# Kernel optimization log

Measured on AMD Instinct MI355X. Metric: run time of the kernel, lower is better.

## Reference

```python
import jax, jax.numpy as jnp
import numpy as np

NUM_HEADS = 4
NUM_GROUPS = 32
EPS = 1e-5


def group_norm(x, gamma, beta):
    B, C, H, W = x.shape
    g = x.reshape(B, NUM_GROUPS, C // NUM_GROUPS, H, W)
    mean = g.mean(axis=(2, 3, 4), keepdims=True)
    var = g.var(axis=(2, 3, 4), keepdims=True)
    g = (g - mean) * jax.lax.rsqrt(var + EPS)
    x = g.reshape(B, C, H, W)
    return x * gamma[None, :, None, None] + beta[None, :, None, None]


def setup_inputs() -> dict:
    key = jax.random.key(0)
    ks = jax.random.split(key, 7)
    B, C, H, W = 16, 256, 32, 32
    x = jax.random.normal(ks[0], (B, C, H, W), dtype=jnp.float32)
    gn_gamma = jnp.ones((C,), dtype=jnp.float32)
    gn_beta = jnp.zeros((C,), dtype=jnp.float32)
    s = 1.0 / np.sqrt(C)
    qkv_w = jax.random.normal(ks[1], (3 * C, C), dtype=jnp.float32) * s
    qkv_b = jnp.zeros((3 * C,), dtype=jnp.float32)
    proj_w = jax.random.normal(ks[2], (C, C), dtype=jnp.float32) * s
    proj_b = jnp.zeros((C,), dtype=jnp.float32)
    return {"x": x, "gn_gamma": gn_gamma, "gn_beta": gn_beta,
            "qkv_w": qkv_w, "qkv_b": qkv_b, "proj_w": proj_w, "proj_b": proj_b}


def reference(x, gn_gamma, gn_beta, qkv_w, qkv_b, proj_w, proj_b):
    B, C, H, W = x.shape
    nh = NUM_HEADS
    d = C // nh
    N = H * W

    h = group_norm(x, gn_gamma, gn_beta)
    # 1x1 conv == channel matmul
    qkv = jnp.einsum('bchw,oc->bohw', h, qkv_w) + qkv_b[None, :, None, None]
    qkv = qkv.reshape(B, 3, nh, d, N)
    q, k, v = qkv[:, 0], qkv[:, 1], qkv[:, 2]  # each [B, nh, d, N]

    scale = 1.0 / jnp.sqrt(jnp.asarray(d, dtype=x.dtype))
    attn = jnp.einsum('bhdn,bhdm->bhnm', q, k) * scale  # [B, nh, N, N]
    attn = jax.nn.softmax(attn, axis=-1)
    out = jnp.einsum('bhnm,bhdm->bhdn', attn, v)  # [B, nh, d, N]
    out = out.reshape(B, C, H, W)

    out = jnp.einsum('bchw,oc->bohw', out, proj_w) + proj_b[None, :, None, None]
    return x + out
```

## Files before the change

### kernel.cpp

```cpp
#include <hip/hip_runtime.h>
#include <math.h>

typedef unsigned short u16;
typedef unsigned int u32;
typedef __attribute__((ext_vector_type(8))) short s16x8;
typedef __attribute__((ext_vector_type(4))) float f32x4;

#define NB 16
#define NN 1024
#define GN_EPS 1e-5f

static __device__ __forceinline__ u16 f2bf(float f) {
    union { float f; u32 u; } v; v.f = f;
    return (u16)((v.u + 0x8000u) >> 16);
}
static __device__ __forceinline__ u32 pk2(float a, float b) {
    union { float f; u32 u; } A, B; A.f = a; B.f = b;
    return __builtin_amdgcn_perm(A.u + 0x8000u, B.u + 0x8000u, 0x03020706u);
}
static __device__ __forceinline__ u32 cvtpk2(float a, float b) {
    u32 r;
    asm("v_cvt_pk_bf16_f32 %0, %1, %2" : "=v"(r) : "v"(a), "v"(b));
    return r;
}

#define GLL16(gp, lp) __builtin_amdgcn_global_load_lds( \
    (const __attribute__((address_space(1))) void*)(const void*)(gp), \
    (__attribute__((address_space(3))) void*)(void*)(lp), 16, 0, 0)

__global__ __launch_bounds__(256) void gn_fused_kernel(
    const float* __restrict__ x, const float* __restrict__ gamma,
    const float* __restrict__ beta, u16* __restrict__ Xtg)
{
    const int gg = blockIdx.x;
    const int b  = blockIdx.y;
    const int t  = threadIdx.x;
    __shared__ float T[8 * 1028];
    __shared__ float red[8];
    __shared__ float sstat[2];

    const float4* xb = (const float4*)(x + ((size_t)b * 32 + gg) * 8192);
    float s = 0.f, ss = 0.f;
#pragma unroll
    for (int i = 0; i < 8; ++i) {
        float4 f = xb[i * 256 + t];
        *(float4*)&T[i * 1028 + t * 4] = f;
        s  += f.x + f.y + f.z + f.w;
        ss += f.x * f.x + f.y * f.y + f.z * f.z + f.w * f.w;
    }
#pragma unroll
    for (int off = 32; off > 0; off >>= 1) {
        s  += __shfl_down(s, off);
        ss += __shfl_down(ss, off);
    }
    if ((t & 63) == 0) { red[t >> 6] = s; red[4 + (t >> 6)] = ss; }
    __syncthreads();
    if (t == 0) {
        float sa = red[0] + red[1] + red[2] + red[3];
        float sb = red[4] + red[5] + red[6] + red[7];
        float mean = sa * (1.0f / 8192.0f);
        float var  = sb * (1.0f / 8192.0f) - mean * mean;
        sstat[0] = mean; sstat[1] = 1.0f / sqrtf(var + GN_EPS);
    }
    __syncthreads();
    const float mean = sstat[0], rstd = sstat[1];
    float gm[8], bt[8];
#pragma unroll
    for (int j = 0; j < 8; ++j) {
        float gj = gamma[gg * 8 + j];
        gm[j] = gj * rstd;
        bt[j] = beta[gg * 8 + j] - mean * rstd * gj;
    }
    u16* dst = Xtg + ((size_t)(b * 32 + gg) * NN) * 8;
#pragma unroll
    for (int rep = 0; rep < 4; ++rep) {
        int n = rep * 256 + t;
        u32 o[4];
#pragma unroll
        for (int p = 0; p < 4; ++p) {
            float v0 = T[(2 * p)     * 1028 + n] * gm[2 * p]     + bt[2 * p];
            float v1 = T[(2 * p + 1) * 1028 + n] * gm[2 * p + 1] + bt[2 * p + 1];
            o[p] = pk2(v0, v1);
        }
        *(uint4*)(dst + (size_t)n * 8) = make_uint4(o[0], o[1], o[2], o[3]);
    }
}

__global__ __launch_bounds__(256) void wcvt_kernel(
    const float* __restrict__ qkv_w, const float* __restrict__ proj_w,
    u16* __restrict__ wqb, u16* __restrict__ wpb)
{
    int i = blockIdx.x * 256 + threadIdx.x;
    if (i < 49152) {
        float4 f = ((const float4*)qkv_w)[i];
        *(uint2*)(wqb + (size_t)i * 4) = make_uint2(pk2(f.x, f.y), pk2(f.z, f.w));
    } else {
        int j = i - 49152;
        float4 f = ((const float4*)proj_w)[j];
        *(uint2*)(wpb + (size_t)j * 4) = make_uint2(pk2(f.x, f.y), pk2(f.z, f.w));
    }
}

__global__ __launch_bounds__(256) void qkv_mfma_kernel(
    const u16* __restrict__ Wb, const float* __restrict__ bias,
    const u16* __restrict__ Xtg,
    u16* __restrict__ qh, u16* __restrict__ kh, u16* __restrict__ vh)
{
    const int b = blockIdx.z, h = blockIdx.y, nt = blockIdx.x;
    const int t = threadIdx.x, w = t >> 6, l = t & 63;
    const int g = l >> 4, c = l & 15;
    __shared__ u16 Slds[32 * 512];
    const u16* Xb = Xtg + (size_t)b * 32 * NN * 8;
    const size_t bhoff = (size_t)(b * 4 + h) << 16;
    const u16* Wq = Wb + (size_t)(h)     * 64 * 256;
    const u16* Wk = Wb + (size_t)(4 + h) * 64 * 256;
    const u16* Wv = Wb + (size_t)(8 + h) * 64 * 256;

#pragma unroll
    for (int s = w; s < 32; s += 4) {
        int osub = s >> 3, ks = s & 7;
        GLL16(Wq + (size_t)(osub * 16 + c) * 256 + ks * 32 + g * 8, Slds + s * 512);
    }
    s16x8 a0[8], a1[8];
#pragma unroll
    for (int ks = 0; ks < 8; ++ks) {
        a0[ks] = *(const s16x8*)(Xb + ((size_t)(ks * 4 + g) * NN + nt * 128 + (2 * w) * 16 + c) * 8);
        a1[ks] = *(const s16x8*)(Xb + ((size_t)(ks * 4 + g) * NN + nt * 128 + (2 * w + 1) * 16 + c) * 8);
    }
    f32x4 acc[2][4];
#pragma unroll
    for (int i = 0; i < 2; ++i)
#pragma unroll
        for (int j = 0; j < 4; ++j) acc[i][j] = (f32x4){0.f, 0.f, 0.f, 0.f};
    __syncthreads();

#pragma unroll
    for (int ks = 0; ks < 8; ++ks)
#pragma unroll
        for (int j = 0; j < 4; ++j) {
            s16x8 bf = *(const s16x8*)(Slds + (j * 8 + ks) * 512 + l * 8);
            acc[0][j] = __builtin_amdgcn_mfma_f32_16x16x32_bf16(a0[ks], bf, acc[0][j], 0, 0, 0);
            acc[1][j] = __builtin_amdgcn_mfma_f32_16x16x32_bf16(a1[ks], bf, acc[1][j], 0, 0, 0);
        }
    __syncthreads();

#pragma unroll
    for (int s = w; s < 32; s += 4) {
        int osub = s >> 3, ks = s & 7;
        GLL16(Wk + (size_t)(osub * 16 + c) * 256 + ks * 32 + g * 8, Slds + s * 512);
    }
    {
        const float sc = 0.125f * 1.44269504088896f;
        float bv[4];
#pragma unroll
        for (int j = 0; j < 4; ++j) bv[j] = bias[h * 64 + j * 16 + c];
        u16* dst = qh + bhoff + (size_t)(nt * 128) * 64;
#pragma unroll
        for (int i = 0; i < 2; ++i)
#pragma unroll
            for (int j = 0; j < 4; ++j)
#pragma unroll
                for (int r = 0; r < 4; ++r) {
                    int n = (2 * w + i) * 16 + g * 4 + r;
                    dst[(size_t)n * 64 + j * 16 + c] = f2bf((acc[i][j][r] + bv[j]) * sc);
                }
    }
#pragma unroll
    for (int i = 0; i < 2; ++i)
#pragma unroll
        for (int j = 0; j < 4; ++j) acc[i][j] = (f32x4){0.f, 0.f, 0.f, 0.f};
    asm volatile("s_waitcnt vmcnt(32)" ::: "memory");
    __builtin_amdgcn_s_barrier();
    asm volatile("" ::: "memory");

#pragma unroll
    for (int ks = 0; ks < 8; ++ks)
#pragma unroll
        for (int j = 0; j < 4; ++j) {
            s16x8 bf = *(const s16x8*)(Slds + (j * 8 + ks) * 512 + l * 8);
            acc[0][j] = __builtin_amdgcn_mfma_f32_16x16x32_bf16(a0[ks], bf, acc[0][j], 0, 0, 0);
            acc[1][j] = __builtin_amdgcn_mfma_f32_16x16x32_bf16(a1[ks], bf, acc[1][j], 0, 0, 0);
        }
    __syncthreads();

#pragma unroll
    for (int s = w; s < 32; s += 4) {
        int osub = s >> 3, ks = s & 7;
        GLL16(Wv + (size_t)(osub * 16 + c) * 256 + ks * 32 + g * 8, Slds + s * 512);
    }
    {
        float bv[4];
#pragma unroll
        for (int j = 0; j < 4; ++j) bv[j] = bias[(4 + h) * 64 + j * 16 + c];
        u16* dst = kh + bhoff + (size_t)(nt * 128) * 64;
#pragma unroll
        for (int i = 0; i < 2; ++i)
#pragma unroll
            for (int j = 0; j < 4; ++j)
#pragma unroll
                for (int r = 0; r < 4; ++r) {
                    int n = (2 * w + i) * 16 + g * 4 + r;
                    dst[(size_t)n * 64 + j * 16 + c] = f2bf(acc[i][j][r] + bv[j]);
                }
    }
    f32x4 vacc[4][2];
#pragma unroll
    for (int osub = 0; osub < 4; ++osub)
#pragma unroll
        for (int i = 0; i < 2; ++i) vacc[osub][i] = (f32x4){0.f, 0.f, 0.f, 0.f};
    asm volatile("s_waitcnt vmcnt(32)" ::: "memory");
    __builtin_amdgcn_s_barrier();
    asm volatile("" ::: "memory");

#pragma unroll
    for (int ks = 0; ks < 8; ++ks)
#pragma unroll
        for (int osub = 0; osub < 4; ++osub) {
            s16x8 wf = *(const s16x8*)(Slds + (osub * 8 + ks) * 512 + l * 8);
            vacc[osub][0] = __builtin_amdgcn_mfma_f32_16x16x32_bf16(wf, a0[ks], vacc[osub][0], 0, 0, 0);
            vacc[osub][1] = __builtin_amdgcn_mfma_f32_16x16x32_bf16(wf, a1[ks], vacc[osub][1], 0, 0, 0);
        }
    {
        u16* dst = vh + bhoff;
#pragma unroll
        for (int osub = 0; osub < 4; ++osub)
#pragma unroll
            for (int r = 0; r < 4; ++r) {
                int d = osub * 16 + g * 4 + r;
                float bi = bias[(8 + h) * 64 + d];
#pragma unroll
                for (int i = 0; i < 2; ++i) {
                    int m = nt * 128 + (2 * w + i) * 16 + c;
                    dst[(size_t)d * NN + m] = f2bf(vacc[osub][i][r] + bi);
                }
            }
    }
}

__global__ __launch_bounds__(512, 4) void attn_mfma_kernel(
    const u16* __restrict__ qh, const u16* __restrict__ kh,
    const u16* __restrict__ vh, u16* __restrict__ aoT)
{
    const int t = threadIdx.x;
    const int w = t >> 6, l = t & 63;
    const int g = l >> 4, c = l & 15;
    const int bid = blockIdx.x;
    const int xcd = bid & 7;
    const int idx = bid >> 3;
    const int qt  = idx & 7;
    const int grp = (idx >> 3) * 8 + xcd;
    const int b = grp >> 2, h = grp & 3;
    const size_t bhoff = (size_t)grp << 16;
    const int n_base = qt * 128 + w * 16;

    __shared__ u16 Klds[4][8 * 512];
    __shared__ u16 Vlds[4][8 * 512];
    __shared__ u16 Plds[8][2 * 512];

    const u16* qb = qh + bhoff;
    const u16* kb = kh + bhoff;
    const u16* vb = vh + bhoff;

    const int msub = w >> 1, uu = w & 1;

    s16x8 qf[2];
#pragma unroll
    for (int u = 0; u < 2; ++u)
        qf[u] = *(const s16x8*)(qb + (size_t)(n_base + c) * 64 + u * 32 + g * 8);

    s16x8 onef;
#pragma unroll
    for (int j = 0; j < 8; ++j) onef[j] = (short)0x3F80;

    f32x4 Oacc[4];
    f32x4 Lacc = (f32x4){0.f, 0.f, 0.f, 0.f};
#pragma unroll
    for (int ds = 0; ds < 4; ++ds) Oacc[ds] = (f32x4){0.f, 0.f, 0.f, 0.f};

    u16* pw = &Plds[w][0];

#define STK(tt) GLL16(kb + (size_t)((tt) * 64 + msub * 16 + c) * 64 + uu * 32 + g * 8, &Klds[(tt) & 3][w * 512])
#define STV(tt) GLL16(vb + (size_t)(msub * 16 + c) * NN + (tt) * 64 + uu * 32 + g * 8, &Vlds[(tt) & 3][w * 512])

    auto tile = [&](int buf) {
        const u16* Kc = &Klds[buf][0];
        const u16* Vc = &Vlds[buf][0];
        f32x4 S[4];
#pragma unroll
        for (int ms = 0; ms < 4; ++ms) S[ms] = (f32x4){0.f, 0.f, 0.f, 0.f};
        __builtin_amdgcn_s_setprio(1);
#pragma unroll
        for (int ms = 0; ms < 4; ++ms)
#pragma unroll
            for (int u = 0; u < 2; ++u) {
                s16x8 af = *(const s16x8*)(Kc + (ms * 2 + u) * 512 + l * 8);
                S[ms] = __builtin_amdgcn_mfma_f32_16x16x32_bf16(af, qf[u], S[ms], 0, 0, 0);
            }
        __builtin_amdgcn_s_setprio(0);
        s16x8 vf[4][2];
#pragma unroll
        for (int ds = 0; ds < 4; ++ds)
#pragma unroll
            for (int u = 0; u < 2; ++u)
                vf[ds][u] = *(const s16x8*)(Vc + (ds * 2 + u) * 512 + l * 8);
#pragma unroll
        for (int ms = 0; ms < 4; ++ms)
#pragma unroll
            for (int r = 0; r < 4; ++r) S[ms][r] = __builtin_amdgcn_exp2f(S[ms][r]);
#pragma unroll
        for (int ms = 0; ms < 4; ++ms) {
            u32 d0 = cvtpk2(S[ms][0], S[ms][1]);
            u32 d1 = cvtpk2(S[ms][2], S[ms][3]);
            int off = (ms >> 1) * 512 + ((ms & 1) * 2 + (g >> 1)) * 128 + c * 8 + (g & 1) * 4;
            *(uint2*)(pw + off) = make_uint2(d0, d1);
        }
        __builtin_amdgcn_s_setprio(1);
#pragma unroll
        for (int u = 0; u < 2; ++u) {
            s16x8 pf = *(const s16x8*)(pw + u * 512 + l * 8);
#pragma unroll
            for (int ds = 0; ds < 4; ++ds)
                Oacc[ds] = __builtin_amdgcn_mfma_f32_16x16x32_bf16(vf[ds][u], pf, Oacc[ds], 0, 0, 0);
            Lacc = __builtin_amdgcn_mfma_f32_16x16x32_bf16(onef, pf, Lacc, 0, 0, 0);
        }
        __builtin_amdgcn_s_setprio(0);
    };

    STK(0); STV(0); STK(1); STV(1);

    for (int it = 0; it < 8; ++it) {
        if (it < 7) {
            STK(2 * it + 2); STV(2 * it + 2);
            STK(2 * it + 3); STV(2 * it + 3);
            asm volatile("s_waitcnt vmcnt(4)" ::: "memory");
        } else {
            asm volatile("s_waitcnt vmcnt(0)" ::: "memory");
        }
        __builtin_amdgcn_s_barrier();
        asm volatile("" ::: "memory");

        tile((2 * it) & 3);
        tile((2 * it + 1) & 3);

        asm volatile("" ::: "memory");
        __builtin_amdgcn_s_barrier();
    }

    u16* aob = aoT + (size_t)b * NN * 256 + h * 64;
    float inv = 1.0f / Lacc[0];
    const size_t nrow = (size_t)(n_base + c) * 256;
#pragma unroll
    for (int ds = 0; ds < 4; ++ds) {
        u32 lo = cvtpk2(Oacc[ds][0] * inv, Oacc[ds][1] * inv);
        u32 hi = cvtpk2(Oacc[ds][2] * inv, Oacc[ds][3] * inv);
        *(uint2*)(aob + nrow + ds * 16 + g * 4) = make_uint2(lo, hi);
    }
#undef STK
#undef STV
}

__global__ __launch_bounds__(256) void proj_mfma_kernel(
    const u16* __restrict__ Wb, const float* __restrict__ bias,
    const u16* __restrict__ aoT, const float* __restrict__ x,
    float* __restrict__ out)
{
    const int b = blockIdx.z, ot = blockIdx.y, nt = blockIdx.x;
    const int t = threadIdx.x, w = t >> 6, l = t & 63;
    const int g = l >> 4, c = l & 15;
    __shared__ u16 Slds[32 * 512];
    const u16* Xb = aoT + ((size_t)b * NN + nt * 128) * 256;
    const u16* Wo = Wb + (size_t)ot * 64 * 256;

    f32x4 acc[8];
#pragma unroll
    for (int j = 0; j < 8; ++j) acc[j] = (f32x4){0.f, 0.f, 0.f, 0.f};
    for (int kk = 0; kk < 256; kk += 128) {
        if (kk) __syncthreads();
#pragma unroll
        for (int s = w; s < 32; s += 4) {
            int nsub = s >> 2, ks = s & 3;
            GLL16(Xb + (size_t)(nsub * 16 + c) * 256 + kk + ks * 32 + g * 8, Slds + s * 512);
        }
        __syncthreads();
#pragma unroll
        for (int ks = 0; ks < 4; ++ks) {
            s16x8 a = *(const s16x8*)(Wo + (size_t)(w * 16 + c) * 256 + kk + ks * 32 + g * 8);
#pragma unroll
            for (int j = 0; j < 8; ++j) {
                s16x8 xf = *(const s16x8*)(Slds + (j * 4 + ks) * 512 + l * 8);
                acc[j] = __builtin_amdgcn_mfma_f32_16x16x32_bf16(a, xf, acc[j], 0, 0, 0);
            }
        }
    }
    float bv[4];
#pragma unroll
    for (int r = 0; r < 4; ++r) bv[r] = bias[ot * 64 + w * 16 + g * 4 + r];
#pragma unroll
    for (int j = 0; j < 8; ++j)
#pragma unroll
        for (int r = 0; r < 4; ++r) {
            int o = ot * 64 + w * 16 + g * 4 + r;
            int n = nt * 128 + j * 16 + c;
            size_t addr = ((size_t)b * 256 + o) * NN + n;
            out[addr] = acc[j][r] + bv[r] + x[addr];
        }
}

extern "C" void kernel_launch(void* const* d_in, const int* in_sizes, int n_in,
                              void* d_out, int out_size, void* d_ws, size_t ws_size,
                              hipStream_t stream)
{
    const float* x      = (const float*)d_in[0];
    const float* gamma  = (const float*)d_in[1];
    const float* beta   = (const float*)d_in[2];
    const float* qkv_w  = (const float*)d_in[3];
    const float* qkv_b  = (const float*)d_in[4];
    const float* proj_w = (const float*)d_in[5];
    const float* proj_b = (const float*)d_in[6];
    float* out = (float*)d_out;

    float* ws = (float*)d_ws;
    u16* Xtg = (u16*)(ws + 1024);
    u16* wqb = Xtg + (size_t)4194304;
    u16* wpb = wqb + (size_t)196608;
    u16* qh  = wpb + (size_t)65536;
    u16* kh  = qh + (size_t)4194304;
    u16* vh  = kh + (size_t)4194304;
    u16* aoT = vh + (size_t)4194304;

    wcvt_kernel<<<dim3(256), 256, 0, stream>>>(qkv_w, proj_w, wqb, wpb);
    gn_fused_kernel<<<dim3(32, NB), 256, 0, stream>>>(x, gamma, beta, Xtg);

    qkv_mfma_kernel<<<dim3(8, 4, NB), 256, 0, stream>>>(
        wqb, qkv_b, Xtg, qh, kh, vh);

    attn_mfma_kernel<<<dim3(512), 512, 0, stream>>>(qh, kh, vh, aoT);

    proj_mfma_kernel<<<dim3(8, 4, NB), 256, 0, stream>>>(
        wpb, proj_b, aoT, x, out);
}
```

Measured before the change: 71.97 us.

## Stage QKV and attention outputs through LDS for coalesced 16-byte global stores

The QKV kernel now writes its bf16 Q, K and V tiles into a per-wave padded LDS buffer and then emits 16-byte vector stores, replacing scattered 2-byte global stores. The attention epilogue does the same via the K LDS region before writing aoT rows, and the projection kernel uses nontemporal stores for the output. The vmcnt wait count is lowered to match the smaller number of outstanding stores. This adds LDS usage and relies on intra-wave ordering of the LDS round trip; it also reuses Klds in attention after the final barrier.

```diff
diff --git a/kernel.cpp b/kernel.cpp
--- a/kernel.cpp
+++ b/kernel.cpp
@@ -110,11 +110,13 @@
     const int t = threadIdx.x, w = t >> 6, l = t & 63;
     const int g = l >> 4, c = l & 15;
     __shared__ u16 Slds[32 * 512];
+    __shared__ u16 Blds[4][2560];
     const u16* Xb = Xtg + (size_t)b * 32 * NN * 8;
     const size_t bhoff = (size_t)(b * 4 + h) << 16;
     const u16* Wq = Wb + (size_t)(h)     * 64 * 256;
     const u16* Wk = Wb + (size_t)(4 + h) * 64 * 256;
     const u16* Wv = Wb + (size_t)(8 + h) * 64 * 256;
+    u16* bw = &Blds[w][0];
 
 #pragma unroll
     for (int s = w; s < 32; s += 4) {
@@ -154,22 +156,30 @@
         float bv[4];
 #pragma unroll
         for (int j = 0; j < 4; ++j) bv[j] = bias[h * 64 + j * 16 + c];
-        u16* dst = qh + bhoff + (size_t)(nt * 128) * 64;
 #pragma unroll
         for (int i = 0; i < 2; ++i)
 #pragma unroll
             for (int j = 0; j < 4; ++j)
 #pragma unroll
-                for (int r = 0; r < 4; ++r) {
-                    int n = (2 * w + i) * 16 + g * 4 + r;
-                    dst[(size_t)n * 64 + j * 16 + c] = f2bf((acc[i][j][r] + bv[j]) * sc);
-                }
+                for (int r = 0; r < 4; ++r)
+                    bw[(i * 16 + g * 4 + r) * 72 + j * 16 + c] = f2bf((acc[i][j][r] + bv[j]) * sc);
+        const int row = l >> 1, half = l & 1;
+        const u16* src = bw + row * 72 + half * 32;
+        u16* dst = qh + bhoff + (size_t)(nt * 128 + w * 32 + row) * 64 + half * 32;
+        s16x8 v0 = *(const s16x8*)(src);
+        s16x8 v1 = *(const s16x8*)(src + 8);
+        s16x8 v2 = *(const s16x8*)(src + 16);
+        s16x8 v3 = *(const s16x8*)(src + 24);
+        *(s16x8*)(dst)      = v0;
+        *(s16x8*)(dst + 8)  = v1;
+        *(s16x8*)(dst + 16) = v2;
+        *(s16x8*)(dst + 24) = v3;
     }
 #pragma unroll
     for (int i = 0; i < 2; ++i)
 #pragma unroll
         for (int j = 0; j < 4; ++j) acc[i][j] = (f32x4){0.f, 0.f, 0.f, 0.f};
-    asm volatile("s_waitcnt vmcnt(32)" ::: "memory");
+    asm volatile("s_waitcnt vmcnt(4)" ::: "memory");
     __builtin_amdgcn_s_barrier();
     asm volatile("" ::: "memory");
 
@@ -192,23 +202,31 @@
         float bv[4];
 #pragma unroll
         for (int j = 0; j < 4; ++j) bv[j] = bias[(4 + h) * 64 + j * 16 + c];
-        u16* dst = kh + bhoff + (size_t)(nt * 128) * 64;
 #pragma unroll
         for (int i = 0; i < 2; ++i)
 #pragma unroll
             for (int j = 0; j < 4; ++j)
 #pragma unroll
-                for (int r = 0; r < 4; ++r) {
-                    int n = (2 * w + i) * 16 + g * 4 + r;
-                    dst[(size_t)n * 64 + j * 16 + c] = f2bf(acc[i][j][r] + bv[j]);
-                }
+                for (int r = 0; r < 4; ++r)
+                    bw[(i * 16 + g * 4 + r) * 72 + j * 16 + c] = f2bf(acc[i][j][r] + bv[j]);
+        const int row = l >> 1, half = l & 1;
+        const u16* src = bw + row * 72 + half * 32;
+        u16* dst = kh + bhoff + (size_t)(nt * 128 + w * 32 + row) * 64 + half * 32;
+        s16x8 v0 = *(const s16x8*)(src);
+        s16x8 v1 = *(const s16x8*)(src + 8);
+        s16x8 v2 = *(const s16x8*)(src + 16);
+        s16x8 v3 = *(const s16x8*)(src + 24);
+        *(s16x8*)(dst)      = v0;
+        *(s16x8*)(dst + 8)  = v1;
+        *(s16x8*)(dst + 16) = v2;
+        *(s16x8*)(dst + 24) = v3;
     }
     f32x4 vacc[4][2];
 #pragma unroll
     for (int osub = 0; osub < 4; ++osub)
 #pragma unroll
         for (int i = 0; i < 2; ++i) vacc[osub][i] = (f32x4){0.f, 0.f, 0.f, 0.f};
-    asm volatile("s_waitcnt vmcnt(32)" ::: "memory");
+    asm volatile("s_waitcnt vmcnt(4)" ::: "memory");
     __builtin_amdgcn_s_barrier();
     asm volatile("" ::: "memory");
 
@@ -221,7 +239,6 @@
             vacc[osub][1] = __builtin_amdgcn_mfma_f32_16x16x32_bf16(wf, a1[ks], vacc[osub][1], 0, 0, 0);
         }
     {
-        u16* dst = vh + bhoff;
 #pragma unroll
         for (int osub = 0; osub < 4; ++osub)
 #pragma unroll
@@ -229,11 +246,19 @@
                 int d = osub * 16 + g * 4 + r;
                 float bi = bias[(8 + h) * 64 + d];
 #pragma unroll
-                for (int i = 0; i < 2; ++i) {
-                    int m = nt * 128 + (2 * w + i) * 16 + c;
-                    dst[(size_t)d * NN + m] = f2bf(vacc[osub][i][r] + bi);
-                }
+                for (int i = 0; i < 2; ++i)
+                    bw[d * 40 + i * 16 + c] = f2bf(vacc[osub][i][r] + bi);
             }
+        const u16* src = bw + l * 40;
+        u16* dst = vh + bhoff + (size_t)l * NN + nt * 128 + w * 32;
+        s16x8 v0 = *(const s16x8*)(src);
+        s16x8 v1 = *(const s16x8*)(src + 8);
+        s16x8 v2 = *(const s16x8*)(src + 16);
+        s16x8 v3 = *(const s16x8*)(src + 24);
+        *(s16x8*)(dst)      = v0;
+        *(s16x8*)(dst + 8)  = v1;
+        *(s16x8*)(dst + 16) = v2;
+        *(s16x8*)(dst + 24) = v3;
     }
 }
 
@@ -346,14 +371,22 @@
         __builtin_amdgcn_s_barrier();
     }
 
-    u16* aob = aoT + (size_t)b * NN * 256 + h * 64;
-    float inv = 1.0f / Lacc[0];
-    const size_t nrow = (size_t)(n_base + c) * 256;
-#pragma unroll
-    for (int ds = 0; ds < 4; ++ds) {
-        u32 lo = cvtpk2(Oacc[ds][0] * inv, Oacc[ds][1] * inv);
-        u32 hi = cvtpk2(Oacc[ds][2] * inv, Oacc[ds][3] * inv);
-        *(uint2*)(aob + nrow + ds * 16 + g * 4) = make_uint2(lo, hi);
+    {
+        u16* ob = ((u16*)Klds) + w * 1152;
+        u32* ob32 = (u32*)ob;
+        float inv = 1.0f / Lacc[0];
+#pragma unroll
+        for (int ds = 0; ds < 4; ++ds) {
+            ob32[(c * 72 + ds * 16 + g * 4) >> 1]     = cvtpk2(Oacc[ds][0] * inv, Oacc[ds][1] * inv);
+            ob32[(c * 72 + ds * 16 + g * 4 + 2) >> 1] = cvtpk2(Oacc[ds][2] * inv, Oacc[ds][3] * inv);
+        }
+        const int n_loc = l >> 2, q4 = l & 3;
+        const u16* src = ob + n_loc * 72 + q4 * 16;
+        u16* dst = aoT + (size_t)b * NN * 256 + (size_t)(n_base + n_loc) * 256 + h * 64 + q4 * 16;
+        s16x8 v0 = *(const s16x8*)(src);
+        s16x8 v1 = *(const s16x8*)(src + 8);
+        *(s16x8*)(dst)     = v0;
+        *(s16x8*)(dst + 8) = v1;
     }
 #undef STK
 #undef STV
@@ -402,7 +435,7 @@
             int o = ot * 64 + w * 16 + g * 4 + r;
             int n = nt * 128 + j * 16 + c;
             size_t addr = ((size_t)b * 256 + o) * NN + n;
-            out[addr] = acc[j][r] + bv[r] + x[addr];
+            __builtin_nontemporal_store(acc[j][r] + bv[r] + x[addr], &out[addr]);
         }
 }
 
```

Result: slower. 76.10 us (+5.7%).
